# Kernel tuning notes

Hardware: AMD Instinct MI355X
Metric: run time of the kernel (lower is better)

Reference implementation:

```python
import jax, jax.numpy as jnp
import numpy as np

# Loihi neuron constants (from netParams['neuron'])
VTH_MANT = 80.0
THETA = VTH_MANT * 64.0          # Loihi threshold = vThMant * 2**6
I_DECAY = 1024.0                 # current decay (of 4096)
V_DECAY = 128.0                  # voltage decay (of 4096)
REF_DELAY = 1.0                  # refractory steps after a spike
W_SCALE = 64.0                   # Loihi weighted-input scaling (2**6)
TAU_RHO = 1.0
POOL_W = 1.1 * VTH_MANT          # slayer pool synapse weight (one spike fires output)


@jax.custom_vjp
def spike(v):
    return (v >= THETA).astype(v.dtype)

def _spike_fwd(v):
    return spike(v), v

def _spike_bwd(v, g):
    # SLAYER surrogate gradient: exponential pdf around threshold
    return (g * jnp.exp(-jnp.abs(v - THETA) / (TAU_RHO * THETA)) / THETA,)

spike.defvjp(_spike_fwd, _spike_bwd)


def loihi_dynamics(wsum):
    """CUBA Loihi LIF over time-leading weighted input wsum: [T, ...] -> spikes [T, ...]."""
    i_dec = (4096.0 - I_DECAY) / 4096.0
    v_dec = (4096.0 - V_DECAY) / 4096.0

    def step(carry, x):
        u, v, ref = carry
        u = i_dec * u + W_SCALE * x                    # synaptic current
        v = jnp.where(ref > 0, 0.0, v_dec * v + u)     # membrane, clamped in refractory
        s = spike(v)
        v = v * (1.0 - s)                              # reset on spike
        ref = jnp.where(s > 0, REF_DELAY, jnp.maximum(ref - 1.0, 0.0))
        return (u, v, ref), s

    z = jnp.zeros_like(wsum[0])
    _, s = jax.lax.scan(step, (z, z, z), wsum)
    return s


def delay_shift(s):
    # slayer.delayShift(spike, 1): shift spike train by 1 timestep (time-leading axis)
    return jnp.concatenate([jnp.zeros_like(s[:1]), s[:-1]], axis=0)


def conv2d_t(x, w, pad):
    # x: [T, B, C, H, W]; fold T into batch for the spatial conv
    T, B, C, H, W = x.shape
    y = jax.lax.conv_general_dilated(
        x.reshape(T * B, C, H, W), w, (1, 1), [(pad, pad), (pad, pad)],
        dimension_numbers=('NCHW', 'OIHW', 'NCHW'))
    return y.reshape(T, B, y.shape[1], y.shape[2], y.shape[3])


def sum_pool(x, k):
    # slayer pool: per-channel sum pooling with fixed synaptic weight POOL_W
    y = jax.lax.reduce_window(x, 0.0, jax.lax.add,
                              (1, 1, 1, k, k), (1, 1, 1, k, k), 'VALID')
    return POOL_W * y


def setup_inputs() -> dict:
    key = jax.random.key(0)
    ks = jax.random.split(key, 6)
    B, C, H, W, T = 48, 4, 26, 26, 128
    # Bernoulli(0.1) spike trains
    spike_input = (jax.random.uniform(ks[0], (B, C, H, W, T)) < 0.1).astype(jnp.float32)
    w_conv1 = jax.random.normal(ks[1], (8, 4, 5, 5), jnp.float32) * 4.0
    w_conv2 = jax.random.normal(ks[2], (16, 8, 3, 3), jnp.float32) * 4.0
    w_conv3 = jax.random.normal(ks[3], (32, 16, 3, 3), jnp.float32) * 4.0
    w_fc1 = jax.random.normal(ks[4], (512, 3 * 3 * 32), jnp.float32) * 4.0
    w_fc2 = jax.random.normal(ks[5], (2, 512), jnp.float32) * 4.0
    return {"spike_input": spike_input, "w_conv1": w_conv1, "w_conv2": w_conv2,
            "w_conv3": w_conv3, "w_fc1": w_fc1, "w_fc2": w_fc2}


def reference(spike_input, w_conv1, w_conv2, w_conv3, w_fc1, w_fc2):
    x = jnp.transpose(spike_input, (4, 0, 1, 2, 3))  # [T, B, C, H, W]

    def block(x, w, pad):
        s = delay_shift(loihi_dynamics(conv2d_t(x, w, pad)))
        s = delay_shift(loihi_dynamics(sum_pool(s, 2)))
        return s  # dropout is identity in eval

    x = block(x, w_conv1, 1)   # 26 -> 24 -> 12
    x = block(x, w_conv2, 1)   # 12 -> 12 -> 6
    x = block(x, w_conv3, 1)   # 6 -> 6 -> 3
    T, B = x.shape[0], x.shape[1]
    x = x.reshape(T, B, -1)    # [T, B, 32*3*3] (C,H,W flatten order matches torch view)
    s = delay_shift(loihi_dynamics(jnp.einsum('tbi,oi->tbo', x, w_fc1)))
    s = delay_shift(loihi_dynamics(jnp.einsum('tbi,oi->tbo', s, w_fc2)))
    return jnp.transpose(s, (1, 2, 0))  # [B, 2, T]
```

## Files before the change

kernel.cpp:

```cpp
#include <hip/hip_runtime.h>


#define THETA 5120.0f

typedef __attribute__((ext_vector_type(8))) short bfrag;
typedef __attribute__((ext_vector_type(4))) float ffrag;

__device__ __forceinline__ float dyn_step(float x, float& u, float& v, float& r) {
#pragma clang fp contract(off)
    u = 0.75f * u + 64.0f * x;
    float vn = 0.96875f * v + u;
    vn = (r > 0.0f) ? 0.0f : vn;
    float s;
    if (vn >= THETA) { s = 1.0f; v = 0.0f; r = 1.0f; }
    else             { s = 0.0f; v = vn; r = fmaxf(r - 1.0f, 0.0f); }
    return s;
}

__device__ __forceinline__ float dpp_add_xor1(float x) {
    int y = __builtin_amdgcn_update_dpp(0, __float_as_int(x), 0xB1, 0xF, 0xF, true);
    return x + __int_as_float(y);
}
__device__ __forceinline__ float dpp_add_xor2(float x) {
    int y = __builtin_amdgcn_update_dpp(0, __float_as_int(x), 0x4E, 0xF, 0xF, true);
    return x + __int_as_float(y);
}

__device__ __forceinline__ unsigned int compress4(unsigned long long x) {
    x &= 0x1111111111111111ull;
    x = (x | (x >> 3))  & 0x0303030303030303ull;
    x = (x | (x >> 6))  & 0x000F000F000F000Full;
    x = (x | (x >> 12)) & 0x000000FF000000FFull;
    x = (x | (x >> 24)) & 0xFFFFull;
    return (unsigned int)x;
}

__device__ __forceinline__ unsigned short f2bf(float f) {
    unsigned int u = __float_as_uint(f);
    unsigned int r = (u + 0x7FFFu + ((u >> 16) & 1u)) >> 16;
    return (unsigned short)r;
}
__device__ __forceinline__ float bf2f(unsigned short b) {
    return __uint_as_float(((unsigned int)b) << 16);
}

__device__ __forceinline__ float f4_elem(float4 v, int j) {
    return (j == 0) ? v.x : (j == 1) ? v.y : (j == 2) ? v.z : v.w;
}

__global__ __launch_bounds__(256) void k_masks(const float* __restrict__ in,
                                               uint2* __restrict__ xb) {
    int wv = blockIdx.x * 4 + (threadIdx.x >> 6);
    int lane = threadIdx.x & 63;
    int y = wv % 26; int r = wv / 26;
    int pr = r & 1; int b = r >> 1;
    int ch = lane >> 5;
    int x = lane & 31;
    int act = x < 26;
    int xc = act ? x : 25;
    const float4* src = (const float4*)(in + (size_t)(((b * 4 + pr * 2 + ch) * 26 + y) * 26 + xc) * 128);
    uint2* dst = xb + ((size_t)b * 2 + pr) * 28 + (y + 1);
    for (int t4 = 0; t4 < 32; ++t4) {
        float4 f = src[t4];
#pragma unroll
        for (int k = 0; k < 4; ++k) {
            float fv = f4_elem(f, k);
            unsigned long long bal = __ballot(act && (fv != 0.0f));
            if (lane == 0) {
                unsigned int lo = ((unsigned int)bal & 0x03FFFFFFu) << 1;
                unsigned int hi = ((unsigned int)(bal >> 32) & 0x03FFFFFFu) << 1;
                dst[(size_t)(t4 * 4 + k) * 2688] = make_uint2(lo, hi);
            }
        }
    }
}

template<int H>
__global__ __launch_bounds__(576) void k_wsum1(const uint2* __restrict__ xb,
                                               const float* __restrict__ w1,
                                               float* __restrict__ ws) {
    __shared__ float wsh[400];
    __shared__ ffrag tbl4[660];
    int tid = threadIdx.x;
    int tch = blockIdx.x & 15;
    int b = blockIdx.x >> 4;
    if (tid < 400) wsh[tid] = w1[H * 400 + tid];
    __syncthreads();
    for (int e = tid; e < 660; e += 576) {
        int ch = e / 165;
        int rem = e % 165;
        int ky = rem / 33;
        int idx = rem % 33;
        ffrag val = {0.f, 0.f, 0.f, 0.f};
#pragma unroll
        for (int oc4 = 0; oc4 < 4; ++oc4) {
            float a = 0.f;
#pragma unroll
            for (int k = 0; k < 5; ++k)
                a += ((idx >> k) & 1) ? wsh[oc4 * 100 + ch * 25 + ky * 5 + k] : 0.f;
            val[oc4] = a;
        }
        tbl4[(ch * 5 + ky) * 33 + idx] = val;
    }
    __syncthreads();
    int q = tid >> 2, s = tid & 3;
    int ox = (q % 12) * 2 + (s & 1);
    int oy = (q / 12) * 2 + (s >> 1);
    int t0 = tch * 8;
    ffrag acc[8];
#pragma unroll
    for (int j = 0; j < 8; ++j) {
        int t = t0 + j;
        const uint2* rp = xb + ((size_t)t * 48 + b) * 56 + oy;
        ffrag a = {0.f, 0.f, 0.f, 0.f};
#pragma unroll
        for (int ky = 0; ky < 5; ++ky) {
            uint2 r0 = rp[ky];
            uint2 r1 = rp[28 + ky];
            a += tbl4[ky * 33 + (int)((r0.x >> ox) & 31u)];
            a += tbl4[(5 + ky) * 33 + (int)((r0.y >> ox) & 31u)];
            a += tbl4[(10 + ky) * 33 + (int)((r1.x >> ox) & 31u)];
            a += tbl4[(15 + ky) * 33 + (int)((r1.y >> ox) & 31u)];
        }
        acc[j] = a;
    }
    size_t tilebase = (size_t)(t0 >> 4) * 1769472 + (t0 & 15);
#pragma unroll
    for (int oc4 = 0; oc4 < 4; ++oc4) {
        float* wp = ws + tilebase + (size_t)((b * 4 + oc4) * 576 + tid) * 16;
        *(float4*)(wp)     = make_float4(acc[0][oc4], acc[1][oc4], acc[2][oc4], acc[3][oc4]);
        *(float4*)(wp + 4) = make_float4(acc[4][oc4], acc[5][oc4], acc[6][oc4], acc[7][oc4]);
    }
}

template<int H>
__global__ __launch_bounds__(256) void k_scan1(const float* __restrict__ ws,
                                               unsigned short* __restrict__ st1) {
    int wv = blockIdx.x * 4 + (threadIdx.x >> 6);
    int lane = threadIdx.x & 63;
    const float* bp = ws + (size_t)(wv * 64 + lane) * 16;
    unsigned short* so = st1 + ((size_t)(H * 1728 + wv)) * 128;
    float u = 0.f, v = 0.f, rf = 0.f;
    float pu = 0.f, pv = 0.f, prf = 0.f;
    float sp = 0.f;
    unsigned int mb[4];
    float4 cur[4], nxt[4];
#pragma unroll
    for (int i = 0; i < 4; ++i) cur[i] = *(const float4*)(bp + i * 4);
    for (int tb = 0; tb < 8; ++tb) {
        if (tb < 7) {
            const float* np = bp + (size_t)(tb + 1) * 1769472;
#pragma unroll
            for (int i = 0; i < 4; ++i) nxt[i] = *(const float4*)(np + i * 4);
        }
#pragma unroll
        for (int j = 0; j < 16; ++j) {
            int t = tb * 16 + j;
            float w = f4_elem(cur[j >> 2], j & 3);
            float cnt = dpp_add_xor2(dpp_add_xor1(sp));
            float ps = dyn_step(88.0f * cnt, pu, pv, prf);
            unsigned long long bal = __ballot(((lane & 3) == 0) && (ps > 0.5f));
            unsigned int m = compress4(bal);
            int sl = (t >> 1) & 3;
            mb[sl] = (t & 1) ? (mb[sl] | (m << 16)) : m;
            if ((t & 7) == 7 && lane == 0)
                *(uint4*)(so + (t & ~7)) = make_uint4(mb[0], mb[1], mb[2], mb[3]);
            sp = dyn_step(w, u, v, rf);
        }
        if (tb < 7) {
#pragma unroll
            for (int i = 0; i < 4; ++i) cur[i] = nxt[i];
        }
    }
}

__global__ __launch_bounds__(256) void k_mb1(const unsigned short* __restrict__ st1,
                                             unsigned short* __restrict__ pb16) {
    int gid = blockIdx.x * 256 + threadIdx.x;
    int oc = gid & 7; int r = gid >> 3;
    int y = r % 12; r /= 12;
    int b = r % 48; int t = r / 48;
    int base = (oc >> 2) * 1728 + (b * 4 + (oc & 3)) * 9;
    int Q0 = y * 12;
    int w0 = Q0 >> 4, off = Q0 & 15;
    unsigned int v0 = st1[(size_t)(base + w0) * 128 + t];
    unsigned int v1 = (off > 4) ? (unsigned int)st1[(size_t)(base + w0 + 1) * 128 + t] : 0u;
    unsigned int m = ((v0 >> off) | (v1 << (16 - off))) & 0xFFFu;
    pb16[((size_t)(t * 48 + b) * 14 + y + 1) * 8 + oc] = (unsigned short)(m << 1);
}

__global__ __launch_bounds__(576) void k_wsum2(const unsigned short* __restrict__ pb16,
                                               const float* __restrict__ w2,
                                               float* __restrict__ ws) {
    __shared__ float wsh[288];
    __shared__ ffrag tbl4[852];
    int tid = threadIdx.x;
    int tch = blockIdx.x & 3;
    int r = blockIdx.x >> 2;
    int ocg = r & 3; int b = r >> 2;
    if (tid < 288) wsh[tid] = w2[(ocg * 4 + tid / 72) * 72 + (tid % 72)];
    __syncthreads();
    for (int e = tid; e < 852; e += 576) {
        int pr = e / 213;
        int rem = e % 213;
        int ky = rem / 71;
        int idx = rem % 71;
        int lo = idx % 9, hi = idx / 9;
        ffrag val = {0.f, 0.f, 0.f, 0.f};
#pragma unroll
        for (int oc4 = 0; oc4 < 4; ++oc4) {
            float a = 0.f;
#pragma unroll
            for (int k = 0; k < 3; ++k)
                a += ((lo >> k) & 1) ? wsh[oc4 * 72 + (2 * pr) * 9 + ky * 3 + k] : 0.f;
#pragma unroll
            for (int k = 0; k < 3; ++k)
                a += ((hi >> k) & 1) ? wsh[oc4 * 72 + (2 * pr + 1) * 9 + ky * 3 + k] : 0.f;
            val[oc4] = a;
        }
        tbl4[(pr * 3 + ky) * 71 + idx] = val;
    }
    __syncthreads();
    int tq = tid / 144;
    int pix = tid % 144;
    int q = pix >> 2, s = pix & 3;
    int ox = (q % 6) * 2 + (s & 1);
    int oy = (q / 6) * 2 + (s >> 1);
    int t0 = tch * 32 + tq * 8;
    ffrag acc[8];
#pragma unroll
    for (int j = 0; j < 8; ++j) {
        int t = t0 + j;
        ffrag a = {0.f, 0.f, 0.f, 0.f};
        if (t > 0) {
            const uint4* rp = (const uint4*)(pb16 + (((size_t)(t - 1) * 48 + b) * 14 + oy) * 8);
#pragma unroll
            for (int ky = 0; ky < 3; ++ky) {
                uint4 row = rp[ky];
                unsigned int wd[4] = {row.x, row.y, row.z, row.w};
#pragma unroll
                for (int pr = 0; pr < 4; ++pr) {
                    unsigned int lo = (wd[pr] >> ox) & 7u;
                    unsigned int hi = (wd[pr] >> (16 + ox)) & 7u;
                    a += tbl4[(pr * 3 + ky) * 71 + (int)(lo + 9u * hi)];
                }
            }
        }
        acc[j] = a;
    }
    size_t tilebase = (size_t)(t0 >> 4) * 1769472 + (t0 & 15);
#pragma unroll
    for (int oc4 = 0; oc4 < 4; ++oc4) {
        int neuron = (b * 16 + ocg * 4 + oc4) * 144 + pix;
        float* wp = ws + tilebase + (size_t)neuron * 16;
        *(float4*)(wp)     = make_float4(acc[0][oc4], acc[1][oc4], acc[2][oc4], acc[3][oc4]);
        *(float4*)(wp + 4) = make_float4(acc[4][oc4], acc[5][oc4], acc[6][oc4], acc[7][oc4]);
    }
}

__global__ __launch_bounds__(576) void k_scan2(const float* __restrict__ ws,
                                               unsigned short* __restrict__ st2) {
    int tid = threadIdx.x;
    int wloc = tid >> 6, lane = tid & 63;
    int g4 = blockIdx.x;
    const float* bp = ws + (size_t)(g4 * 576 + tid) * 16;
    unsigned short* so = st2 + ((size_t)(g4 * 9 + wloc)) * 128;
    float u = 0.f, v = 0.f, rf = 0.f;
    float pu = 0.f, pv = 0.f, prf = 0.f;
    float sp = 0.f;
    unsigned int mb[4];
    float4 cur[4], nxt[4];
#pragma unroll
    for (int i = 0; i < 4; ++i) cur[i] = *(const float4*)(bp + i * 4);
    for (int tb = 0; tb < 8; ++tb) {
        if (tb < 7) {
            const float* np = bp + (size_t)(tb + 1) * 1769472;
#pragma unroll
            for (int i = 0; i < 4; ++i) nxt[i] = *(const float4*)(np + i * 4);
        }
#pragma unroll
        for (int j = 0; j < 16; ++j) {
            int t = tb * 16 + j;
            float w = f4_elem(cur[j >> 2], j & 3);
            float cnt = dpp_add_xor2(dpp_add_xor1(sp));
            float ps = dyn_step(88.0f * cnt, pu, pv, prf);
            unsigned long long bal = __ballot(((lane & 3) == 0) && (ps > 0.5f));
            unsigned int m = compress4(bal);
            int sl = (t >> 1) & 3;
            mb[sl] = (t & 1) ? (mb[sl] | (m << 16)) : m;
            if ((t & 7) == 7 && lane == 0)
                *(uint4*)(so + (t & ~7)) = make_uint4(mb[0], mb[1], mb[2], mb[3]);
            sp = dyn_step(w, u, v, rf);
        }
        if (tb < 7) {
#pragma unroll
            for (int i = 0; i < 4; ++i) cur[i] = nxt[i];
        }
    }
}

__global__ __launch_bounds__(256) void k_mb2(const unsigned short* __restrict__ st2,
                                             unsigned short* __restrict__ pb2) {
    int gid = blockIdx.x * 256 + threadIdx.x;
    int oc = gid & 15; int r = gid >> 4;
    int y = r % 6; r /= 6;
    int b = r % 48; int t = r / 48;
    int img = b * 16 + oc;
    int g4 = img >> 2, lI = img & 3;
    int Q0 = lI * 36 + y * 6;
    int w0 = Q0 >> 4, off = Q0 & 15;
    unsigned int v0 = st2[(size_t)(g4 * 9 + w0) * 128 + t];
    unsigned int v1 = (off > 10) ? (unsigned int)st2[(size_t)(g4 * 9 + w0 + 1) * 128 + t] : 0u;
    unsigned int m = ((v0 >> off) | (v1 << (16 - off))) & 0x3Fu;
    pb2[((size_t)(t * 48 + b) * 8 + y + 1) * 16 + oc] = (unsigned short)(m << 1);
}

__global__ __launch_bounds__(576) void k_wsum3(const unsigned short* __restrict__ pb2,
                                               const float* __restrict__ w3,
                                               float* __restrict__ ws) {
    __shared__ float wsh[576];
    __shared__ ffrag tbl4[1704];
    int tid = threadIdx.x;
    int tch = blockIdx.x & 7;
    int gb = blockIdx.x >> 3;
    int ocg = gb / 12, bg = gb % 12;
    wsh[tid] = w3[(ocg * 4 + tid / 144) * 144 + (tid % 144)];
    __syncthreads();
    for (int e = tid; e < 1536; e += 576) {
        int pr = e / 192;
        int ky = (e / 64) % 3;
        int i = e & 63;
        int lo = i & 7, hi = i >> 3;
        ffrag val = {0.f, 0.f, 0.f, 0.f};
#pragma unroll
        for (int oc4 = 0; oc4 < 4; ++oc4) {
            float a = 0.f;
#pragma unroll
            for (int k = 0; k < 3; ++k)
                a += ((lo >> k) & 1) ? wsh[oc4 * 144 + (2 * pr) * 9 + ky * 3 + k] : 0.f;
#pragma unroll
            for (int k = 0; k < 3; ++k)
                a += ((hi >> k) & 1) ? wsh[oc4 * 144 + (2 * pr + 1) * 9 + ky * 3 + k] : 0.f;
            val[oc4] = a;
        }
        tbl4[(pr * 3 + ky) * 71 + lo + 9 * hi] = val;
    }
    __syncthreads();
    int tq = tid & 3;
    int r = tid >> 2;
    int pix = r % 36;
    int bsel = r / 36;
    int q = pix >> 2, s = pix & 3;
    int ox = (q % 3) * 2 + (s & 1);
    int oy = (q / 3) * 2 + (s >> 1);
    int b = bg * 4 + bsel;
    int t0 = tch * 16 + tq * 4;
    ffrag acc[4];
#pragma unroll
    for (int j = 0; j < 4; ++j) {
        int t = t0 + j;
        ffrag a = {0.f, 0.f, 0.f, 0.f};
        if (t > 0) {
            const uint4* rp = (const uint4*)(pb2 + (((size_t)(t - 1) * 48 + b) * 8 + oy) * 16);
#pragma unroll
            for (int ky = 0; ky < 3; ++ky) {
                uint4 rA = rp[ky * 2];
                uint4 rB = rp[ky * 2 + 1];
                unsigned int wd[8] = {rA.x, rA.y, rA.z, rA.w, rB.x, rB.y, rB.z, rB.w};
#pragma unroll
                for (int pr = 0; pr < 8; ++pr) {
                    unsigned int lo = (wd[pr] >> ox) & 7u;
                    unsigned int hi = (wd[pr] >> (16 + ox)) & 7u;
                    a += tbl4[(pr * 3 + ky) * 71 + (int)(lo + 9u * hi)];
                }
            }
        }
        acc[j] = a;
    }
    size_t base = (size_t)tch * 884736;
#pragma unroll
    for (int oc4 = 0; oc4 < 4; ++oc4) {
        int neuron = (b * 32 + ocg * 4 + oc4) * 36 + pix;
        float* wp = ws + base + (size_t)neuron * 16 + tq * 4;
        *(float4*)(wp) = make_float4(acc[0][oc4], acc[1][oc4], acc[2][oc4], acc[3][oc4]);
    }
}

__global__ __launch_bounds__(256) void k_scan3(const float* __restrict__ ws,
                                               unsigned short* __restrict__ st3) {
    int wv = blockIdx.x * 4 + (threadIdx.x >> 6);
    int lane = threadIdx.x & 63;
    const float* bp = ws + (size_t)(wv * 64 + lane) * 16;
    unsigned short* so = st3 + (size_t)wv * 128;
    float u = 0.f, v = 0.f, rf = 0.f;
    float pu = 0.f, pv = 0.f, prf = 0.f;
    float sp = 0.f;
    unsigned int mb[4];
    float4 cur[4], nxt[4];
#pragma unroll
    for (int i = 0; i < 4; ++i) cur[i] = *(const float4*)(bp + i * 4);
    for (int tb = 0; tb < 8; ++tb) {
        if (tb < 7) {
            const float* np = bp + (size_t)(tb + 1) * 884736;
#pragma unroll
            for (int i = 0; i < 4; ++i) nxt[i] = *(const float4*)(np + i * 4);
        }
#pragma unroll
        for (int j = 0; j < 16; ++j) {
            int t = tb * 16 + j;
            float w = f4_elem(cur[j >> 2], j & 3);
            float cnt = dpp_add_xor2(dpp_add_xor1(sp));
            float ps = dyn_step(88.0f * cnt, pu, pv, prf);
            unsigned long long bal = __ballot(((lane & 3) == 0) && (ps > 0.5f));
            unsigned int m = compress4(bal);
            int sl = (t >> 1) & 3;
            mb[sl] = (t & 1) ? (mb[sl] | (m << 16)) : m;
            if ((t & 7) == 7 && lane == 0)
                *(uint4*)(so + (t & ~7)) = make_uint4(mb[0], mb[1], mb[2], mb[3]);
            sp = dyn_step(w, u, v, rf);
        }
        if (tb < 7) {
#pragma unroll
            for (int i = 0; i < 4; ++i) cur[i] = nxt[i];
        }
    }
}

__global__ __launch_bounds__(256) void k_mb3(const unsigned short* __restrict__ st3,
                                             unsigned short* __restrict__ a3) {
    int gid = blockIdx.x * 256 + threadIdx.x;
    if (gid >= 1755648) return;
    int G = gid % 13824, t = gid / 13824;
    unsigned int bit = ((unsigned int)st3[(size_t)(G >> 4) * 128 + t] >> (G & 15)) & 1u;
    a3[(size_t)(t + 1) * 13824 + G] = bit ? 0x3F80 : 0;
}

__global__ __launch_bounds__(256) void k_wsplit(const float* __restrict__ wfc1,
                                                unsigned short* __restrict__ wb) {
    int gid = blockIdx.x * 256 + threadIdx.x;
    int o = gid / 288, k = gid % 288;
    float w = wfc1[gid];
    unsigned short b0 = f2bf(w);
    float r1 = w - bf2f(b0);
    unsigned short b1 = f2bf(r1);
    float r2 = r1 - bf2f(b1);
    unsigned short b2 = f2bf(r2);
    wb[(size_t)k * 512 + o] = b0;
    wb[(size_t)147456 + k * 512 + o] = b1;
    wb[(size_t)294912 + k * 512 + o] = b2;
}

__global__ __launch_bounds__(256) void k_fc1mm(const unsigned short* __restrict__ a3,
                                               const unsigned short* __restrict__ wb,
                                               float* __restrict__ wsf1) {
    __shared__ unsigned short Bs[16 * 872];
    int tid = threadIdx.x;
    int nt = blockIdx.x & 31;
    int mc = blockIdx.x >> 5;
    int n0 = nt * 16;
    for (int idx = tid; idx < 13824; idx += 256) {
        int kp = idx >> 4;
        int n = idx & 15;
        Bs[n * 872 + kp] = wb[(size_t)kp * 512 + n0 + n];
    }
    __syncthreads();
    int wave = tid >> 6;
    int lane = tid & 63;
    int ln = lane & 15, quad = lane >> 4;
#pragma unroll
    for (int i = 0; i < 4; ++i) {
        int m0 = (mc * 16 + wave * 4 + i) * 16;
        const unsigned short* arow = a3 + (size_t)(m0 + ln) * 288 + quad * 8;
        ffrag acc = {0.f, 0.f, 0.f, 0.f};
#pragma unroll
        for (int kb = 0; kb < 9; ++kb) {
            bfrag av = *(const bfrag*)(arow + kb * 32);
#pragma unroll
            for (int c = 0; c < 3; ++c) {
                bfrag bv = *(const bfrag*)(&Bs[ln * 872 + c * 288 + kb * 32 + quad * 8]);
                acc = __builtin_amdgcn_mfma_f32_16x16x32_bf16(av, bv, acc, 0, 0, 0);
            }
        }
        float* wout = wsf1 + (size_t)(m0 + quad * 4) * 512 + n0 + ln;
        wout[0] = acc[0];
        wout[512] = acc[1];
        wout[1024] = acc[2];
        wout[1536] = acc[3];
    }
}

__global__ __launch_bounds__(256) void k_fc1s(const float* __restrict__ wsf1,
                                              float* __restrict__ f1f) {
    int tid = blockIdx.x * 256 + threadIdx.x;
    float u = 0.f, v = 0.f, rf = 0.f;
    float wbuf[16];
#pragma unroll
    for (int i = 0; i < 16; ++i) wbuf[i] = wsf1[(size_t)i * 24576 + tid];
    for (int tb = 0; tb < 128; tb += 16) {
#pragma unroll
        for (int j = 0; j < 16; ++j) {
            int t = tb + j;
            float w = wbuf[j];
            if (t + 16 < 128) wbuf[j] = wsf1[(size_t)(t + 16) * 24576 + tid];
            float s = dyn_step(w, u, v, rf);
            f1f[(size_t)t * 24576 + tid] = s;
        }
    }
}

__global__ __launch_bounds__(256) void k_fc2w(const float* __restrict__ f1f,
                                              const float* __restrict__ wfc2,
                                              float* __restrict__ wsf2) {
    int wv = blockIdx.x * 4 + (threadIdx.x >> 6);
    int lane = threadIdx.x & 63;
    int b = wv % 48, t = wv / 48;
    int o = lane & 1, kq = lane >> 1;
    float acc = 0.f;
    if (t > 0) {
        const float* wp = wfc2 + o * 512 + kq * 16;
        const float* sp = f1f + (size_t)(t - 1) * 24576 + b * 512 + kq * 16;
#pragma unroll
        for (int i = 0; i < 16; ++i) acc += wp[i] * sp[i];
    }
#pragma unroll
    for (int m = 2; m < 64; m <<= 1) acc += __shfl_xor(acc, m, 64);
    if (lane < 2) wsf2[(size_t)t * 96 + b * 2 + o] = acc;
}

__global__ __launch_bounds__(128) void k_fc2s(const float* __restrict__ wsf2,
                                              float* __restrict__ out) {
    int tid = threadIdx.x;
    if (tid >= 96) return;
    float* ob = out + tid * 128;
    ob[0] = 0.0f;
    float u = 0.f, v = 0.f, rf = 0.f;
    float wbuf[8];
#pragma unroll
    for (int i = 0; i < 8; ++i) wbuf[i] = wsf2[(size_t)i * 96 + tid];
    for (int tb = 0; tb < 128; tb += 8) {
#pragma unroll
        for (int j = 0; j < 8; ++j) {
            int t = tb + j;
            float w = wbuf[j];
            if (t + 8 < 128) wbuf[j] = wsf2[(size_t)(t + 8) * 96 + tid];
            float s = dyn_step(w, u, v, rf);
            if (t < 127) ob[t + 1] = s;
        }
    }
}

extern "C" void kernel_launch(void* const* d_in, const int* in_sizes, int n_in,
                              void* d_out, int out_size, void* d_ws, size_t ws_size,
                              hipStream_t stream) {
    const float* in   = (const float*)d_in[0];
    const float* w1   = (const float*)d_in[1];
    const float* w2   = (const float*)d_in[2];
    const float* w3   = (const float*)d_in[3];
    const float* wfc1 = (const float*)d_in[4];
    const float* wfc2 = (const float*)d_in[5];
    float* out = (float*)d_out;
    char* ws = (char*)d_ws;

    float*          slab = (float*)(ws);
    uint2*          xb   = (uint2*)(ws + 56623104);
    unsigned short* pb16 = (unsigned short*)(ws + 59375616);
    unsigned short* pb2  = (unsigned short*)(ws + 60751872);
    float*          f1f  = (float*)(ws + 64094208);
    unsigned short* a3   = (unsigned short*)(ws + 76677120);
    unsigned short* wb   = (unsigned short*)(ws + 80216064);
    unsigned short* st1  = (unsigned short*)(ws + 81100800);
    unsigned short* st2  = (unsigned short*)(ws + 81985536);
    unsigned short* st3  = (unsigned short*)(ws + 82427904);
    float*          wsf1 = (float*)(ws);
    float*          wsf2 = (float*)(ws + 16777216);

    hipMemsetAsync(xb, 0, 2752512, stream);
    hipMemsetAsync(pb16, 0, 1376256, stream);
    hipMemsetAsync(pb2, 0, 1572864, stream);
    hipMemsetAsync(a3, 0, 27648, stream);

    k_wsplit  <<<576, 256, 0, stream>>>(wfc1, wb);
    k_masks   <<<624, 256, 0, stream>>>(in, xb);
    k_wsum1<0><<<768, 576, 0, stream>>>(xb, w1, slab);
    k_scan1<0><<<432, 256, 0, stream>>>(slab, st1);
    k_wsum1<1><<<768, 576, 0, stream>>>(xb, w1, slab);
    k_scan1<1><<<432, 256, 0, stream>>>(slab, st1);
    k_mb1     <<<2304, 256, 0, stream>>>(st1, pb16);
    k_wsum2   <<<768, 576, 0, stream>>>(pb16, w2, slab);
    k_scan2   <<<192, 576, 0, stream>>>(slab, st2);
    k_mb2     <<<2304, 256, 0, stream>>>(st2, pb2);
    k_wsum3   <<<768, 576, 0, stream>>>(pb2, w3, slab);
    k_scan3   <<<216, 256, 0, stream>>>(slab, st3);
    k_mb3     <<<6858, 256, 0, stream>>>(st3, a3);
    k_fc1mm   <<<768, 256, 0, stream>>>(a3, wb, wsf1);
    k_fc1s    <<<96, 256, 0, stream>>>(wsf1, f1f);
    k_fc2w    <<<1536, 256, 0, stream>>>(f1f, wfc2, wsf2);
    k_fc2s    <<<1, 128, 0, stream>>>(wsf2, out);
}
```

Measured before the change: 397.9 us.

## Merge the two conv1 channel-half passes into one wsum and scan launch

Conv1 was previously computed in two halves of 4 output channels, each with its own wsum and scan launch. Now one wsum kernel computes all 8 channels, reusing each decoded input bitmask index for both channel halves, over 4 timesteps per block instead of 8. The scan kernel runs once over twice as many waves with a remapped output index. The slab doubles in size, so the other workspace buffers shift, and the larger LUT build per block adds shared-memory setup.

```diff
diff --git a/kernel.cpp b/kernel.cpp
--- a/kernel.cpp
+++ b/kernel.cpp
@@ -75,71 +75,83 @@
     }
 }
 
-template<int H>
 __global__ __launch_bounds__(576) void k_wsum1(const uint2* __restrict__ xb,
                                                const float* __restrict__ w1,
                                                float* __restrict__ ws) {
-    __shared__ float wsh[400];
-    __shared__ ffrag tbl4[660];
+    __shared__ float wsh[800];
+    __shared__ ffrag tbl4[1320];
     int tid = threadIdx.x;
-    int tch = blockIdx.x & 15;
-    int b = blockIdx.x >> 4;
-    if (tid < 400) wsh[tid] = w1[H * 400 + tid];
+    int tch = blockIdx.x & 31;
+    int b = blockIdx.x >> 5;
+    for (int e = tid; e < 800; e += 576) wsh[e] = w1[e];
     __syncthreads();
-    for (int e = tid; e < 660; e += 576) {
-        int ch = e / 165;
-        int rem = e % 165;
-        int ky = rem / 33;
-        int idx = rem % 33;
+    for (int e = tid; e < 1320; e += 576) {
+        int quad = e / 660;
+        int rem = e % 660;
+        int ch = rem / 165;
+        int rem2 = rem % 165;
+        int ky = rem2 / 33;
+        int idx = rem2 % 33;
         ffrag val = {0.f, 0.f, 0.f, 0.f};
 #pragma unroll
         for (int oc4 = 0; oc4 < 4; ++oc4) {
             float a = 0.f;
 #pragma unroll
             for (int k = 0; k < 5; ++k)
-                a += ((idx >> k) & 1) ? wsh[oc4 * 100 + ch * 25 + ky * 5 + k] : 0.f;
+                a += ((idx >> k) & 1) ? wsh[(quad * 4 + oc4) * 100 + ch * 25 + ky * 5 + k] : 0.f;
             val[oc4] = a;
         }
-        tbl4[(ch * 5 + ky) * 33 + idx] = val;
+        tbl4[(quad * 20 + ch * 5 + ky) * 33 + idx] = val;
     }
     __syncthreads();
     int q = tid >> 2, s = tid & 3;
     int ox = (q % 12) * 2 + (s & 1);
     int oy = (q / 12) * 2 + (s >> 1);
-    int t0 = tch * 8;
-    ffrag acc[8];
-#pragma unroll
-    for (int j = 0; j < 8; ++j) {
+    int t0 = tch * 4;
+    ffrag accA[4], accB[4];
+#pragma unroll
+    for (int j = 0; j < 4; ++j) {
         int t = t0 + j;
         const uint2* rp = xb + ((size_t)t * 48 + b) * 56 + oy;
         ffrag a = {0.f, 0.f, 0.f, 0.f};
+        ffrag c = {0.f, 0.f, 0.f, 0.f};
 #pragma unroll
         for (int ky = 0; ky < 5; ++ky) {
             uint2 r0 = rp[ky];
             uint2 r1 = rp[28 + ky];
-            a += tbl4[ky * 33 + (int)((r0.x >> ox) & 31u)];
-            a += tbl4[(5 + ky) * 33 + (int)((r0.y >> ox) & 31u)];
-            a += tbl4[(10 + ky) * 33 + (int)((r1.x >> ox) & 31u)];
-            a += tbl4[(15 + ky) * 33 + (int)((r1.y >> ox) & 31u)];
-        }
-        acc[j] = a;
-    }
-    size_t tilebase = (size_t)(t0 >> 4) * 1769472 + (t0 & 15);
+            int w0 = (int)((r0.x >> ox) & 31u);
+            int w1i = (int)((r0.y >> ox) & 31u);
+            int w2 = (int)((r1.x >> ox) & 31u);
+            int w3 = (int)((r1.y >> ox) & 31u);
+            a += tbl4[ky * 33 + w0];
+            a += tbl4[(5 + ky) * 33 + w1i];
+            a += tbl4[(10 + ky) * 33 + w2];
+            a += tbl4[(15 + ky) * 33 + w3];
+            c += tbl4[(20 + ky) * 33 + w0];
+            c += tbl4[(25 + ky) * 33 + w1i];
+            c += tbl4[(30 + ky) * 33 + w2];
+            c += tbl4[(35 + ky) * 33 + w3];
+        }
+        accA[j] = a; accB[j] = c;
+    }
+    size_t base = (size_t)(tch >> 2) * 3538944 + (tch & 3) * 4;
 #pragma unroll
     for (int oc4 = 0; oc4 < 4; ++oc4) {
-        float* wp = ws + tilebase + (size_t)((b * 4 + oc4) * 576 + tid) * 16;
-        *(float4*)(wp)     = make_float4(acc[0][oc4], acc[1][oc4], acc[2][oc4], acc[3][oc4]);
-        *(float4*)(wp + 4) = make_float4(acc[4][oc4], acc[5][oc4], acc[6][oc4], acc[7][oc4]);
-    }
-}
-
-template<int H>
+        float* wpA = ws + base + (size_t)((b * 8 + oc4) * 576 + tid) * 16;
+        *(float4*)wpA = make_float4(accA[0][oc4], accA[1][oc4], accA[2][oc4], accA[3][oc4]);
+        float* wpB = ws + base + (size_t)((b * 8 + 4 + oc4) * 576 + tid) * 16;
+        *(float4*)wpB = make_float4(accB[0][oc4], accB[1][oc4], accB[2][oc4], accB[3][oc4]);
+    }
+}
+
 __global__ __launch_bounds__(256) void k_scan1(const float* __restrict__ ws,
                                                unsigned short* __restrict__ st1) {
     int wv = blockIdx.x * 4 + (threadIdx.x >> 6);
     int lane = threadIdx.x & 63;
     const float* bp = ws + (size_t)(wv * 64 + lane) * 16;
-    unsigned short* so = st1 + ((size_t)(H * 1728 + wv)) * 128;
+    int img8 = wv / 9, sub = wv % 9;
+    int b = img8 >> 3, oc = img8 & 7;
+    unsigned short* so = st1 + ((size_t)((oc >> 2) * 1728 + (b * 4 + (oc & 3)) * 9 + sub)) * 128;
     float u = 0.f, v = 0.f, rf = 0.f;
     float pu = 0.f, pv = 0.f, prf = 0.f;
     float sp = 0.f;
@@ -149,7 +161,7 @@
     for (int i = 0; i < 4; ++i) cur[i] = *(const float4*)(bp + i * 4);
     for (int tb = 0; tb < 8; ++tb) {
         if (tb < 7) {
-            const float* np = bp + (size_t)(tb + 1) * 1769472;
+            const float* np = bp + (size_t)(tb + 1) * 3538944;
 #pragma unroll
             for (int i = 0; i < 4; ++i) nxt[i] = *(const float4*)(np + i * 4);
         }
@@ -562,15 +574,15 @@
     char* ws = (char*)d_ws;
 
     float*          slab = (float*)(ws);
-    uint2*          xb   = (uint2*)(ws + 56623104);
-    unsigned short* pb16 = (unsigned short*)(ws + 59375616);
-    unsigned short* pb2  = (unsigned short*)(ws + 60751872);
-    float*          f1f  = (float*)(ws + 64094208);
-    unsigned short* a3   = (unsigned short*)(ws + 76677120);
-    unsigned short* wb   = (unsigned short*)(ws + 80216064);
-    unsigned short* st1  = (unsigned short*)(ws + 81100800);
-    unsigned short* st2  = (unsigned short*)(ws + 81985536);
-    unsigned short* st3  = (unsigned short*)(ws + 82427904);
+    uint2*          xb   = (uint2*)(ws + 113246208);
+    unsigned short* pb16 = (unsigned short*)(ws + 115998720);
+    unsigned short* pb2  = (unsigned short*)(ws + 117374976);
+    float*          f1f  = (float*)(ws + 118947840);
+    unsigned short* a3   = (unsigned short*)(ws + 131530752);
+    unsigned short* wb   = (unsigned short*)(ws + 135069696);
+    unsigned short* st1  = (unsigned short*)(ws + 135954432);
+    unsigned short* st2  = (unsigned short*)(ws + 136839168);
+    unsigned short* st3  = (unsigned short*)(ws + 137281536);
     float*          wsf1 = (float*)(ws);
     float*          wsf2 = (float*)(ws + 16777216);
 
@@ -581,10 +593,8 @@
 
     k_wsplit  <<<576, 256, 0, stream>>>(wfc1, wb);
     k_masks   <<<624, 256, 0, stream>>>(in, xb);
-    k_wsum1<0><<<768, 576, 0, stream>>>(xb, w1, slab);
-    k_scan1<0><<<432, 256, 0, stream>>>(slab, st1);
-    k_wsum1<1><<<768, 576, 0, stream>>>(xb, w1, slab);
-    k_scan1<1><<<432, 256, 0, stream>>>(slab, st1);
+    k_wsum1   <<<1536, 576, 0, stream>>>(xb, w1, slab);
+    k_scan1   <<<864, 256, 0, stream>>>(slab, st1);
     k_mb1     <<<2304, 256, 0, stream>>>(st1, pb16);
     k_wsum2   <<<768, 576, 0, stream>>>(pb16, w2, slab);
     k_scan2   <<<192, 576, 0, stream>>>(slab, st2);
```

After: 419.5 us. 1.05x slower.
